# Optimization experiments

Hardware: AMD Instinct MI355X
Metric: run time of the kernel (lower is better)

The kernel has to match this reference:

```python
import jax, jax.numpy as jnp
import numpy as np

T, B, NI, NH = 512, 64, 1024, 1024
SIGMA = 0.01

def setup_inputs() -> dict:
    key = jax.random.key(0)
    ks = jax.random.split(key, 9)
    inputs = jax.random.normal(ks[0], (T, B, NI), dtype=jnp.float32)
    def w(k, shape):
        return jax.random.normal(k, shape, dtype=jnp.float32) * SIGMA
    return {
        "inputs": inputs,
        "W_xf": w(ks[1], (NI, NH)), "W_hf": w(ks[2], (NH, NH)), "b_f": jnp.zeros((NH,), jnp.float32),
        "W_xi": w(ks[3], (NI, NH)), "W_hi": w(ks[4], (NH, NH)), "b_i": jnp.zeros((NH,), jnp.float32),
        "W_xc": w(ks[5], (NI, NH)), "W_hc": w(ks[6], (NH, NH)), "b_c": jnp.zeros((NH,), jnp.float32),
        "W_xo": w(ks[7], (NI, NH)), "W_ho": w(ks[8], (NH, NH)), "b_o": jnp.zeros((NH,), jnp.float32),
    }

def reference(inputs, W_xf, W_hf, b_f, W_xi, W_hi, b_i, W_xc, W_hc, b_c, W_xo, W_ho, b_o):
    # Precompute input projections for all 4 gates in one batched GEMM each:
    # [T,B,NI] @ [NI,4*NH] -> [T,B,4*NH]
    W_x = jnp.concatenate([W_xf, W_xi, W_xc, W_xo], axis=1)
    W_h = jnp.concatenate([W_hf, W_hi, W_hc, W_ho], axis=1)
    b = jnp.concatenate([b_f, b_i, b_c, b_o])
    x_proj = jnp.einsum('tbi,ih->tbh', inputs, W_x) + b  # [T,B,4*NH]

    H0 = jnp.zeros((inputs.shape[1], W_hf.shape[0]), inputs.dtype)
    C0 = jnp.zeros_like(H0)

    def step(carry, xp):
        H, C = carry
        gates = xp + H @ W_h  # [B, 4*NH]
        f, i, c_t, o = jnp.split(gates, 4, axis=-1)
        F = jax.nn.sigmoid(f)
        I = jax.nn.sigmoid(i)
        C_tilde = jnp.tanh(c_t)
        O = jax.nn.sigmoid(o)
        C_new = F * C + I * C_tilde
        H_new = O * jnp.tanh(C_new)
        return (H_new, C_new), H_new

    (H, C), outputs = jax.lax.scan(step, (H0, C0), x_proj)
    return outputs, (H, C)
```

## Files before the change

### kernel.cpp

```cpp
#include <hip/hip_runtime.h>
#include <hip/hip_bf16.h>

#define TT  512
#define BB  64
#define NII 1024
#define NHH 1024
#define NBLK 256

typedef __attribute__((ext_vector_type(8))) short bf16x8;
typedef __attribute__((ext_vector_type(4))) float f32x4;
typedef unsigned long long u64;

#define WPK_BYTES  (16ull << 20)
#define FLG_BYTES  (16384ull)
#define HPP_BYTES  (256ull << 10)
#define XPK_BYTES  (64ull << 20)
#define GX_BYTES   (256ull << 20)
#define HBUF_SHORTS 32768ull

#define MFMA16 __builtin_amdgcn_mfma_f32_16x16x32_bf16
#define LD_AG(p)    __hip_atomic_load((p),  __ATOMIC_RELAXED, __HIP_MEMORY_SCOPE_AGENT)
#define ST_AG(p, v) __hip_atomic_store((p), (v), __ATOMIC_RELAXED, __HIP_MEMORY_SCOPE_AGENT)

__device__ __forceinline__ float fast_sigmoid(float x) {
    return __builtin_amdgcn_rcpf(1.0f + __expf(-x));
}
__device__ __forceinline__ float fast_tanh(float x) {
    float e = __expf(2.0f * x);
    return 1.0f - 2.0f * __builtin_amdgcn_rcpf(e + 1.0f);
}
__device__ __forceinline__ short f2bf(float f) {
    union { __hip_bfloat16 b; short s; } u; u.b = __float2bfloat16(f); return u.s;
}
__device__ __forceinline__ float bf2f(short h) {
    union { unsigned u; float f; } v; v.u = ((unsigned)(unsigned short)h) << 16; return v.f;
}

__device__ __forceinline__ bf16x8 ld_coh16(const short* p) {
    const u64* q = (const u64*)p;
    u64 a = LD_AG(q);
    u64 b = LD_AG(q + 1);
    union { u64 u[2]; bf16x8 v; } u;
    u.u[0] = a; u.u[1] = b; return u.v;
}

__global__ __launch_bounds__(256)
void pack_weights_kernel(const float* __restrict__ Wxf, const float* __restrict__ Whf,
                         const float* __restrict__ Wxi, const float* __restrict__ Whi,
                         const float* __restrict__ Wxc, const float* __restrict__ Whc,
                         const float* __restrict__ Wxo, const float* __restrict__ Who,
                         short* __restrict__ wpk)
{
    const int c = blockIdx.x;
    const int t = threadIdx.x;
    const float* Wx[4] = { Wxf, Wxi, Wxc, Wxo };
    const float* Wh[4] = { Whf, Whi, Whc, Who };

    for (int i = 0; i < 32; ++i) {
        const int d   = t + i * 256;
        const int kkf = d >> 7;
        const int nt  = (d >> 6) & 1;
        const int l   = d & 63;
        const int n   = nt * 16 + (l & 15);
        const int g   = n >> 3;
        const int col = c * 8 + (n & 7);
        const int kf0 = kkf * 32 + (l >> 4) * 8;
        const float* src = (kf0 < 1024) ? (Wx[g] + (size_t)kf0 * NHH + col)
                                        : (Wh[g] + (size_t)(kf0 - 1024) * NHH + col);
        short v[8];
        #pragma unroll
        for (int e = 0; e < 8; ++e) v[e] = f2bf(src[(size_t)e * NHH]);
        *reinterpret_cast<bf16x8*>(wpk + ((size_t)c * 8192 + d) * 8) =
            *reinterpret_cast<bf16x8*>(v);
    }
}

__global__ __launch_bounds__(256)
void pack_x_kernel(const float* __restrict__ x, short* __restrict__ xpk)
{
    const int t = blockIdx.x;
    const float* xt = x + (size_t)t * BB * NII;
    short* dst = xpk + (size_t)t * 65536;

    for (int i = 0; i < 32; ++i) {
        const int d  = threadIdx.x + i * 256;
        const int s  = d >> 12;
        const int mi = (d >> 11) & 1;
        const int kk = (d >> 6) & 31;
        const int l  = d & 63;
        const int m  = s * 32 + mi * 16 + (l & 15);
        const int k0 = kk * 32 + ((l >> 4) << 3);
        const float* sp = xt + (size_t)m * NII + k0;
        f32x4 a0 = *reinterpret_cast<const f32x4*>(sp);
        f32x4 a1 = *reinterpret_cast<const f32x4*>(sp + 4);
        short v[8];
        #pragma unroll
        for (int e = 0; e < 4; ++e) { v[e] = f2bf(a0[e]); v[4 + e] = f2bf(a1[e]); }
        *reinterpret_cast<bf16x8*>(dst + (size_t)d * 8) = *reinterpret_cast<bf16x8*>(v);
    }
}

__global__ __launch_bounds__(256)
void xproj_gemm(const short* __restrict__ xpk, const short* __restrict__ wpk,
                short* __restrict__ gx)
{
    __shared__ short lds_wx[32768];

    const int tid = threadIdx.x;
    const int w = tid >> 6, l = tid & 63;
    const int cp = blockIdx.x & 127, tg = blockIdx.x >> 7;
    const int s = w >> 1, mi = w & 1;

    const short* src = wpk + (size_t)cp * 65536;
    #pragma unroll
    for (int i = 0; i < 16; ++i) {
        const int ch = tid + i * 256;
        *reinterpret_cast<bf16x8*>(&lds_wx[(size_t)ch * 8]) =
            *reinterpret_cast<const bf16x8*>(&src[(size_t)ch * 8]);
    }
    __syncthreads();

    for (int tt = 0; tt < 64; ++tt) {
        const int t = tg * 64 + tt;
        const short* ap = xpk + (size_t)t * 65536
                        + ((size_t)((s * 2 + mi) * 32) * 64 + l) * 8;
        f32x4 a00 = {0,0,0,0}, a01 = {0,0,0,0}, a10 = {0,0,0,0}, a11 = {0,0,0,0};
        const short* wl = &lds_wx[(size_t)l * 8];
        #pragma unroll 4
        for (int kk = 0; kk < 32; kk += 2) {
            bf16x8 A0  = *reinterpret_cast<const bf16x8*>(ap);
            bf16x8 B00 = *reinterpret_cast<const bf16x8*>(wl);
            bf16x8 B01 = *reinterpret_cast<const bf16x8*>(wl + 512);
            bf16x8 A1  = *reinterpret_cast<const bf16x8*>(ap + 512);
            bf16x8 B10 = *reinterpret_cast<const bf16x8*>(wl + 1024);
            bf16x8 B11 = *reinterpret_cast<const bf16x8*>(wl + 1536);
            a00 = MFMA16(A0, B00, a00, 0, 0, 0);
            a01 = MFMA16(A0, B01, a01, 0, 0, 0);
            a10 = MFMA16(A1, B10, a10, 0, 0, 0);
            a11 = MFMA16(A1, B11, a11, 0, 0, 0);
            ap += 1024; wl += 2048;
        }
        short o[8];
        o[0] = f2bf(a00[0] + a10[0]); o[1] = f2bf(a00[1] + a10[1]);
        o[2] = f2bf(a00[2] + a10[2]); o[3] = f2bf(a00[3] + a10[3]);
        o[4] = f2bf(a01[0] + a11[0]); o[5] = f2bf(a01[1] + a11[1]);
        o[6] = f2bf(a01[2] + a11[2]); o[7] = f2bf(a01[3] + a11[3]);
        short* dst = gx + ((((size_t)t * 2 + s) * 128 + cp) * 2 + mi) * 512
                   + (size_t)l * 8;
        *reinterpret_cast<bf16x8*>(dst) = *reinterpret_cast<bf16x8*>(o);
    }
}

__device__ __forceinline__ void compute_x_half(
    int t, int mi, int l, int s, int use_xpk,
    const float* __restrict__ x, const short* __restrict__ xpk,
    const short* lds_w, float* rdst)
{
    f32x4 a00 = {0,0,0,0}, a01 = {0,0,0,0}, a10 = {0,0,0,0}, a11 = {0,0,0,0};
    const short* wl = lds_w + (size_t)l * 8;
    if (use_xpk) {
        const short* ap = xpk + (size_t)t * 65536
                        + (((size_t)(s * 2 + mi)) * 32) * 512 + (size_t)l * 8;
        #pragma unroll 4
        for (int kk = 0; kk < 32; kk += 2) {
            bf16x8 A0  = *reinterpret_cast<const bf16x8*>(ap);
            bf16x8 B00 = *reinterpret_cast<const bf16x8*>(wl);
            bf16x8 B01 = *reinterpret_cast<const bf16x8*>(wl + 512);
            bf16x8 A1  = *reinterpret_cast<const bf16x8*>(ap + 512);
            bf16x8 B10 = *reinterpret_cast<const bf16x8*>(wl + 1024);
            bf16x8 B11 = *reinterpret_cast<const bf16x8*>(wl + 1536);
            a00 = MFMA16(A0, B00, a00, 0, 0, 0);
            a01 = MFMA16(A0, B01, a01, 0, 0, 0);
            a10 = MFMA16(A1, B10, a10, 0, 0, 0);
            a11 = MFMA16(A1, B11, a11, 0, 0, 0);
            ap += 1024; wl += 2048;
        }
    } else {
        const float* apf = x + ((size_t)t * BB + (size_t)(s * 32 + mi * 16 + (l & 15))) * NII
                         + ((l >> 4) << 3);
        #pragma unroll 4
        for (int kk = 0; kk < 32; kk += 2) {
            f32x4 f0 = *reinterpret_cast<const f32x4*>(apf);
            f32x4 f1 = *reinterpret_cast<const f32x4*>(apf + 4);
            bf16x8 B00 = *reinterpret_cast<const bf16x8*>(wl);
            bf16x8 B01 = *reinterpret_cast<const bf16x8*>(wl + 512);
            f32x4 f2 = *reinterpret_cast<const f32x4*>(apf + 32);
            f32x4 f3 = *reinterpret_cast<const f32x4*>(apf + 36);
            bf16x8 B10 = *reinterpret_cast<const bf16x8*>(wl + 1024);
            bf16x8 B11 = *reinterpret_cast<const bf16x8*>(wl + 1536);
            bf16x8 A0, A1;
            A0[0]=f2bf(f0[0]); A0[1]=f2bf(f0[1]); A0[2]=f2bf(f0[2]); A0[3]=f2bf(f0[3]);
            A0[4]=f2bf(f1[0]); A0[5]=f2bf(f1[1]); A0[6]=f2bf(f1[2]); A0[7]=f2bf(f1[3]);
            A1[0]=f2bf(f2[0]); A1[1]=f2bf(f2[1]); A1[2]=f2bf(f2[2]); A1[3]=f2bf(f2[3]);
            A1[4]=f2bf(f3[0]); A1[5]=f2bf(f3[1]); A1[6]=f2bf(f3[2]); A1[7]=f2bf(f3[3]);
            a00 = MFMA16(A0, B00, a00, 0, 0, 0);
            a01 = MFMA16(A0, B01, a01, 0, 0, 0);
            a10 = MFMA16(A1, B10, a10, 0, 0, 0);
            a11 = MFMA16(A1, B11, a11, 0, 0, 0);
            apf += 64; wl += 2048;
        }
    }
    rdst[0] = a00[0] + a10[0]; rdst[1] = a00[1] + a10[1];
    rdst[2] = a00[2] + a10[2]; rdst[3] = a00[3] + a10[3];
    rdst[4] = a01[0] + a11[0]; rdst[5] = a01[1] + a11[1];
    rdst[6] = a01[2] + a11[2]; rdst[7] = a01[3] + a11[3];
}

__global__ __launch_bounds__(256, 1)
void lstm_persistent(const float* __restrict__ x,
                     const short* __restrict__ xpk,
                     const short* __restrict__ wpk,
                     const short* __restrict__ gx,
                     const float* __restrict__ bfv, const float* __restrict__ biv,
                     const float* __restrict__ bcv, const float* __restrict__ bov,
                     float* __restrict__ out,
                     short* hpp,
                     short* ring,
                     unsigned* flags,
                     int mode)
{
    __shared__ short lds_w[64 * 2 * 64 * 8];
    __shared__ float redx[2][2][64][8];
    __shared__ float redh[4][64][8];
    __shared__ short hstage[256];
    __shared__ int   lds_epoch;

    const int tid = threadIdx.x;
    const int w   = tid >> 6;
    const int l   = tid & 63;
    const int c   = blockIdx.x >> 1;
    const int s   = blockIdx.x & 1;

    unsigned* flags_s = flags + s * 2048;

    if (mode == 2) {
        const short* wsrc = wpk + (size_t)c * 65536 + 32768;
        #pragma unroll
        for (int i = 0; i < 16; ++i) {
            const int ch = tid + i * 256;
            *reinterpret_cast<bf16x8*>(&lds_w[(size_t)ch * 8]) =
                *reinterpret_cast<const bf16x8*>(&wsrc[(size_t)ch * 8]);
        }
    } else {
        const short* wsrc = wpk + (size_t)c * 65536;
        #pragma unroll
        for (int i = 0; i < 32; ++i) {
            const int ch = tid + i * 256;
            *reinterpret_cast<bf16x8*>(&lds_w[(size_t)ch * 8]) =
                *reinterpret_cast<const bf16x8*>(&wsrc[(size_t)ch * 8]);
        }
    }
    if (tid == 0) lds_epoch = -1;

    const int m_loc = tid >> 3;
    const int jc    = tid & 7;
    const int mi2   = m_loc >> 4, ml = m_loc & 15;
    const int lb    = (ml >> 2) << 4, lr = ml & 3;
    const int jcol  = c * 8 + jc;
    const int mrow  = s * 32 + m_loc;
    int lanes[4], es[4];
    #pragma unroll
    for (int g = 0; g < 4; ++g) { lanes[g] = lb + (g & 1) * 8 + jc; es[g] = (g >> 1) * 4 + lr; }

    float B4[4];
    B4[0] = bfv[jcol]; B4[1] = biv[jcol]; B4[2] = bcv[jcol]; B4[3] = bov[jcol];
    float cstate = 0.0f;
    __syncthreads();

    float gxv[4] = {0.f, 0.f, 0.f, 0.f};
    if (mode == 2) {
        const short* gsl = gx + ((((size_t)0 * 2 + s) * 128 + c) * 2 + mi2) * 512;
        #pragma unroll
        for (int g = 0; g < 4; ++g) gxv[g] = bf2f(gsl[(size_t)lanes[g] * 8 + es[g]]);
    } else if (w < 2) {
        compute_x_half(0, w & 1, l, s, mode, x, xpk, lds_w, &redx[0][w & 1][l][0]);
    }

    #pragma unroll 1
    for (int t = 0; t < TT; ++t) {
        const short* rcur = (mode == 2)
            ? ring + (size_t)t * 65536 + (size_t)s * 32768
            : hpp + ((size_t)((t & 1) * 2 + s)) * HBUF_SHORTS;
        short* rnxt = (mode == 2)
            ? ring + (size_t)(t + 1) * 65536 + (size_t)s * 32768
            : hpp + ((size_t)(((t + 1) & 1) * 2 + s)) * HBUF_SHORTS;

        if (mode == 2) {
            if (w == 2) {
                const unsigned tv = (unsigned)t;
                for (;;) {
                    unsigned v0 = LD_AG(flags_s + (size_t)l * 16);
                    unsigned v1 = LD_AG(flags_s + (size_t)(l + 64) * 16);
                    if (__all((v0 >= tv) & (v1 >= tv))) break;
                    __builtin_amdgcn_s_sleep(1);
                }
                if (l == 0) *((volatile int*)&lds_epoch) = t;
            } else {
                while (*((volatile int*)&lds_epoch) < t) { }
            }
            asm volatile("" ::: "memory");

            const int mi = w & 1, ki = w >> 1;
            f32x4 a00 = {0,0,0,0}, a01 = {0,0,0,0}, a10 = {0,0,0,0}, a11 = {0,0,0,0};
            const short* ap = rcur + ((size_t)(mi * 32 + ki * 16) * 64 + l) * 8;
            const short* wl = &lds_w[(size_t)ki * 16384 + (size_t)l * 8];
            #pragma unroll 4
            for (int kk = 0; kk < 16; kk += 2) {
                bf16x8 A0  = *reinterpret_cast<const bf16x8*>(ap);
                bf16x8 B00 = *reinterpret_cast<const bf16x8*>(wl);
                bf16x8 B01 = *reinterpret_cast<const bf16x8*>(wl + 512);
                bf16x8 A1  = *reinterpret_cast<const bf16x8*>(ap + 512);
                bf16x8 B10 = *reinterpret_cast<const bf16x8*>(wl + 1024);
                bf16x8 B11 = *reinterpret_cast<const bf16x8*>(wl + 1536);
                a00 = MFMA16(A0, B00, a00, 0, 0, 0);
                a01 = MFMA16(A0, B01, a01, 0, 0, 0);
                a10 = MFMA16(A1, B10, a10, 0, 0, 0);
                a11 = MFMA16(A1, B11, a11, 0, 0, 0);
                ap += 1024; wl += 2048;
            }
            float* r = &redh[w][l][0];
            r[0] = a00[0] + a10[0]; r[1] = a00[1] + a10[1];
            r[2] = a00[2] + a10[2]; r[3] = a00[3] + a10[3];
            r[4] = a01[0] + a11[0]; r[5] = a01[1] + a11[1];
            r[6] = a01[2] + a11[2]; r[7] = a01[3] + a11[3];
        } else if (w >= 2) {
            const int mi = w & 1;
            if (mi == 0) {
                const unsigned tv = (unsigned)t;
                for (;;) {
                    unsigned v0 = LD_AG(flags_s + (size_t)l * 16);
                    unsigned v1 = LD_AG(flags_s + (size_t)(l + 64) * 16);
                    if (__all((v0 >= tv) & (v1 >= tv))) break;
                    __builtin_amdgcn_s_sleep(1);
                }
                if (l == 0) *((volatile int*)&lds_epoch) = t;
            } else {
                while (*((volatile int*)&lds_epoch) < t) { }
            }
            asm volatile("" ::: "memory");

            f32x4 a00 = {0,0,0,0}, a01 = {0,0,0,0}, a10 = {0,0,0,0}, a11 = {0,0,0,0};
            const short* ap = rcur + ((size_t)(mi * 32)) * 512 + (size_t)l * 8;
            const short* wl = &lds_w[(size_t)32768 + (size_t)l * 8];
            #pragma unroll 4
            for (int kk = 0; kk < 32; kk += 2) {
                bf16x8 A0  = ld_coh16(ap);
                bf16x8 B00 = *reinterpret_cast<const bf16x8*>(wl);
                bf16x8 B01 = *reinterpret_cast<const bf16x8*>(wl + 512);
                bf16x8 A1  = ld_coh16(ap + 512);
                bf16x8 B10 = *reinterpret_cast<const bf16x8*>(wl + 1024);
                bf16x8 B11 = *reinterpret_cast<const bf16x8*>(wl + 1536);
                a00 = MFMA16(A0, B00, a00, 0, 0, 0);
                a01 = MFMA16(A0, B01, a01, 0, 0, 0);
                a10 = MFMA16(A1, B10, a10, 0, 0, 0);
                a11 = MFMA16(A1, B11, a11, 0, 0, 0);
                ap += 1024; wl += 2048;
            }
            float* r = &redh[2 + mi][l][0];
            r[0] = a00[0] + a10[0]; r[1] = a00[1] + a10[1];
            r[2] = a00[2] + a10[2]; r[3] = a00[3] + a10[3];
            r[4] = a01[0] + a11[0]; r[5] = a01[1] + a11[1];
            r[6] = a01[2] + a11[2]; r[7] = a01[3] + a11[3];
        } else {
            if (t + 1 < TT)
                compute_x_half(t + 1, w & 1, l, s, mode, x, xpk, lds_w,
                               &redx[(t + 1) & 1][w & 1][l][0]);
        }
        __syncthreads();

        float gv[4];
        #pragma unroll
        for (int g = 0; g < 4; ++g) {
            const int lane = lanes[g], e = es[g];
            float xterm = (mode == 2) ? (gxv[g] + redh[mi2][lane][e])
                                      : redx[t & 1][mi2][lane][e];
            gv[g] = xterm + redh[2 + mi2][lane][e] + B4[g];
        }
        const float F  = fast_sigmoid(gv[0]);
        const float I  = fast_sigmoid(gv[1]);
        const float Ct = fast_tanh(gv[2]);
        const float O  = fast_sigmoid(gv[3]);
        cstate = F * cstate + I * Ct;
        const float hn = O * fast_tanh(cstate);
        hstage[tid] = f2bf(hn);
        __syncthreads();

        if (w == 0 && t < TT - 1) {
            if (l < 32) {
                const int mi3 = l >> 4, ml3 = l & 15;
                const u64 v0 = ((const u64*)hstage)[l * 2];
                const u64 v1 = ((const u64*)hstage)[l * 2 + 1];
                const size_t sh = ((size_t)(mi3 * 32 + (c >> 2)) * 64
                                   + (size_t)((c & 3) * 16 + ml3)) * 8;
                u64* dq = (u64*)(rnxt + sh);
                ST_AG(dq, v0);
                ST_AG(dq + 1, v1);
            }
            asm volatile("s_waitcnt vmcnt(0)" ::: "memory");
            if (tid == 0)
                ST_AG(&flags_s[(size_t)c * 16], (unsigned)(t + 1));
        }

        __builtin_nontemporal_store(hn, &out[(size_t)t * BB * NHH + (size_t)mrow * NHH + jcol]);
        if (t == TT - 1) {
            float* tail = out + (size_t)TT * BB * NHH;
            tail[(size_t)mrow * NHH + jcol]                    = hn;
            tail[(size_t)BB * NHH + (size_t)mrow * NHH + jcol] = cstate;
        }

        if (mode == 2 && t + 1 < TT) {
            const short* gsl = gx + ((((size_t)(t + 1) * 2 + s) * 128 + c) * 2 + mi2) * 512;
            #pragma unroll
            for (int g = 0; g < 4; ++g) gxv[g] = bf2f(gsl[(size_t)lanes[g] * 8 + es[g]]);
        }
    }
}

extern "C" void kernel_launch(void* const* d_in, const int* in_sizes, int n_in,
                              void* d_out, int out_size, void* d_ws, size_t ws_size,
                              hipStream_t stream) {
    const float* inputs = (const float*)d_in[0];
    const float* Wxf = (const float*)d_in[1],  *Whf = (const float*)d_in[2],  *bf = (const float*)d_in[3];
    const float* Wxi = (const float*)d_in[4],  *Whi = (const float*)d_in[5],  *bi = (const float*)d_in[6];
    const float* Wxc = (const float*)d_in[7],  *Whc = (const float*)d_in[8],  *bc = (const float*)d_in[9];
    const float* Wxo = (const float*)d_in[10], *Who = (const float*)d_in[11], *bo = (const float*)d_in[12];

    float* out = (float*)d_out;
    char*  wsb = (char*)d_ws;

    short*    wpk   = (short*)wsb;
    unsigned* flags = (unsigned*)(wsb + WPK_BYTES);
    short*    hpp   = (short*)(wsb + WPK_BYTES + FLG_BYTES);
    short*    xpk   = (short*)(wsb + WPK_BYTES + FLG_BYTES + HPP_BYTES);
    short*    gx    = (short*)(wsb + WPK_BYTES + FLG_BYTES + HPP_BYTES + XPK_BYTES);

    const size_t needT1 = WPK_BYTES + FLG_BYTES + HPP_BYTES + XPK_BYTES;
    const size_t needT0 = needT1 + GX_BYTES;
    const int mode = (ws_size >= needT0) ? 2 : (ws_size >= needT1) ? 1 : 0;

    hipMemsetAsync(flags, 0, FLG_BYTES + HPP_BYTES, stream);

    pack_weights_kernel<<<dim3(128), dim3(256), 0, stream>>>(
        Wxf, Whf, Wxi, Whi, Wxc, Whc, Wxo, Who, wpk);

    if (mode >= 1)
        pack_x_kernel<<<dim3(TT), dim3(256), 0, stream>>>(inputs, xpk);

    if (mode == 2) {
        xproj_gemm<<<dim3(1024), dim3(256), 0, stream>>>(xpk, wpk, gx);
        hipMemsetAsync(xpk, 0, 131072, stream);
    }

    lstm_persistent<<<dim3(NBLK), dim3(256), 0, stream>>>(
        inputs, xpk, wpk, gx, bf, bi, bc, bo, out, hpp, xpk , flags, mode);
}
```

Measured before the change: 2.754 ms.

## Fuse input projection into persistent LSTM kernel with 8-step lookahead ring

Removes the separate xproj_gemm pass and its large gx buffer. The persistent kernel instead computes the input projection for step t+8 after each recurrent step, using all four waves, global-memory W_x slices and an 8-deep LDS ring placed after the weights. The h ring moves into its own workspace region instead of reusing xpk, so mode 2 now needs a smaller workspace. The aim is to hide the x-projection GEMM inside slack in the latency-bound recurrence. The cost is extra per-step work on the serial critical path and global-memory weight reads, since W_x is not held in LDS.

```diff
diff --git a/kernel.cpp b/kernel.cpp
--- a/kernel.cpp
+++ b/kernel.cpp
@@ -15,7 +15,7 @@
 #define FLG_BYTES  (16384ull)
 #define HPP_BYTES  (256ull << 10)
 #define XPK_BYTES  (64ull << 20)
-#define GX_BYTES   (256ull << 20)
+#define RING_BYTES (64ull << 20)
 #define HBUF_SHORTS 32768ull
 
 #define MFMA16 __builtin_amdgcn_mfma_f32_16x16x32_bf16
@@ -31,9 +31,6 @@
 }
 __device__ __forceinline__ short f2bf(float f) {
     union { __hip_bfloat16 b; short s; } u; u.b = __float2bfloat16(f); return u.s;
-}
-__device__ __forceinline__ float bf2f(short h) {
-    union { unsigned u; float f; } v; v.u = ((unsigned)(unsigned short)h) << 16; return v.f;
 }
 
 __device__ __forceinline__ bf16x8 ld_coh16(const short* p) {
@@ -97,57 +94,6 @@
         #pragma unroll
         for (int e = 0; e < 4; ++e) { v[e] = f2bf(a0[e]); v[4 + e] = f2bf(a1[e]); }
         *reinterpret_cast<bf16x8*>(dst + (size_t)d * 8) = *reinterpret_cast<bf16x8*>(v);
-    }
-}
-
-__global__ __launch_bounds__(256)
-void xproj_gemm(const short* __restrict__ xpk, const short* __restrict__ wpk,
-                short* __restrict__ gx)
-{
-    __shared__ short lds_wx[32768];
-
-    const int tid = threadIdx.x;
-    const int w = tid >> 6, l = tid & 63;
-    const int cp = blockIdx.x & 127, tg = blockIdx.x >> 7;
-    const int s = w >> 1, mi = w & 1;
-
-    const short* src = wpk + (size_t)cp * 65536;
-    #pragma unroll
-    for (int i = 0; i < 16; ++i) {
-        const int ch = tid + i * 256;
-        *reinterpret_cast<bf16x8*>(&lds_wx[(size_t)ch * 8]) =
-            *reinterpret_cast<const bf16x8*>(&src[(size_t)ch * 8]);
-    }
-    __syncthreads();
-
-    for (int tt = 0; tt < 64; ++tt) {
-        const int t = tg * 64 + tt;
-        const short* ap = xpk + (size_t)t * 65536
-                        + ((size_t)((s * 2 + mi) * 32) * 64 + l) * 8;
-        f32x4 a00 = {0,0,0,0}, a01 = {0,0,0,0}, a10 = {0,0,0,0}, a11 = {0,0,0,0};
-        const short* wl = &lds_wx[(size_t)l * 8];
-        #pragma unroll 4
-        for (int kk = 0; kk < 32; kk += 2) {
-            bf16x8 A0  = *reinterpret_cast<const bf16x8*>(ap);
-            bf16x8 B00 = *reinterpret_cast<const bf16x8*>(wl);
-            bf16x8 B01 = *reinterpret_cast<const bf16x8*>(wl + 512);
-            bf16x8 A1  = *reinterpret_cast<const bf16x8*>(ap + 512);
-            bf16x8 B10 = *reinterpret_cast<const bf16x8*>(wl + 1024);
-            bf16x8 B11 = *reinterpret_cast<const bf16x8*>(wl + 1536);
-            a00 = MFMA16(A0, B00, a00, 0, 0, 0);
-            a01 = MFMA16(A0, B01, a01, 0, 0, 0);
-            a10 = MFMA16(A1, B10, a10, 0, 0, 0);
-            a11 = MFMA16(A1, B11, a11, 0, 0, 0);
-            ap += 1024; wl += 2048;
-        }
-        short o[8];
-        o[0] = f2bf(a00[0] + a10[0]); o[1] = f2bf(a00[1] + a10[1]);
-        o[2] = f2bf(a00[2] + a10[2]); o[3] = f2bf(a00[3] + a10[3]);
-        o[4] = f2bf(a01[0] + a11[0]); o[5] = f2bf(a01[1] + a11[1]);
-        o[6] = f2bf(a01[2] + a11[2]); o[7] = f2bf(a01[3] + a11[3]);
-        short* dst = gx + ((((size_t)t * 2 + s) * 128 + cp) * 2 + mi) * 512
-                   + (size_t)l * 8;
-        *reinterpret_cast<bf16x8*>(dst) = *reinterpret_cast<bf16x8*>(o);
     }
 }
 
@@ -206,11 +152,39 @@
     rdst[6] = a01[2] + a11[2]; rdst[7] = a01[3] + a11[3];
 }
 
+__device__ __forceinline__ void compute_x_ki(
+    int t, int mi, int ki, int l, int s,
+    const short* __restrict__ xpk, const short* __restrict__ wxc,
+    float* rdst)
+{
+    f32x4 a00 = {0,0,0,0}, a01 = {0,0,0,0}, a10 = {0,0,0,0}, a11 = {0,0,0,0};
+    const short* ap = xpk + (size_t)t * 65536
+                    + ((size_t)((s * 2 + mi) * 32 + ki * 16)) * 512 + (size_t)l * 8;
+    const short* wl = wxc + (size_t)ki * 16384 + (size_t)l * 8;
+    #pragma unroll 4
+    for (int kk = 0; kk < 16; kk += 2) {
+        bf16x8 A0  = *reinterpret_cast<const bf16x8*>(ap);
+        bf16x8 B00 = *reinterpret_cast<const bf16x8*>(wl);
+        bf16x8 B01 = *reinterpret_cast<const bf16x8*>(wl + 512);
+        bf16x8 A1  = *reinterpret_cast<const bf16x8*>(ap + 512);
+        bf16x8 B10 = *reinterpret_cast<const bf16x8*>(wl + 1024);
+        bf16x8 B11 = *reinterpret_cast<const bf16x8*>(wl + 1536);
+        a00 = MFMA16(A0, B00, a00, 0, 0, 0);
+        a01 = MFMA16(A0, B01, a01, 0, 0, 0);
+        a10 = MFMA16(A1, B10, a10, 0, 0, 0);
+        a11 = MFMA16(A1, B11, a11, 0, 0, 0);
+        ap += 1024; wl += 2048;
+    }
+    rdst[0] = a00[0] + a10[0]; rdst[1] = a00[1] + a10[1];
+    rdst[2] = a00[2] + a10[2]; rdst[3] = a00[3] + a10[3];
+    rdst[4] = a01[0] + a11[0]; rdst[5] = a01[1] + a11[1];
+    rdst[6] = a01[2] + a11[2]; rdst[7] = a01[3] + a11[3];
+}
+
 __global__ __launch_bounds__(256, 1)
 void lstm_persistent(const float* __restrict__ x,
                      const short* __restrict__ xpk,
                      const short* __restrict__ wpk,
-                     const short* __restrict__ gx,
                      const float* __restrict__ bfv, const float* __restrict__ biv,
                      const float* __restrict__ bcv, const float* __restrict__ bov,
                      float* __restrict__ out,
@@ -228,10 +202,14 @@
     const int tid = threadIdx.x;
     const int w   = tid >> 6;
     const int l   = tid & 63;
+    const int mi  = w & 1;
+    const int ki  = w >> 1;
     const int c   = blockIdx.x >> 1;
     const int s   = blockIdx.x & 1;
 
     unsigned* flags_s = flags + s * 2048;
+    float (*redxr)[4][64][8] = (float (*)[4][64][8])(lds_w + 32768);
+    const short* wxc = wpk + (size_t)c * 65536;
 
     if (mode == 2) {
         const short* wsrc = wpk + (size_t)c * 65536 + 32768;
@@ -267,14 +245,13 @@
     float cstate = 0.0f;
     __syncthreads();
 
-    float gxv[4] = {0.f, 0.f, 0.f, 0.f};
     if (mode == 2) {
-        const short* gsl = gx + ((((size_t)0 * 2 + s) * 128 + c) * 2 + mi2) * 512;
-        #pragma unroll
-        for (int g = 0; g < 4; ++g) gxv[g] = bf2f(gsl[(size_t)lanes[g] * 8 + es[g]]);
+        for (int tp = 0; tp < 8; ++tp)
+            compute_x_ki(tp, mi, ki, l, s, xpk, wxc, &redxr[tp][w][l][0]);
     } else if (w < 2) {
-        compute_x_half(0, w & 1, l, s, mode, x, xpk, lds_w, &redx[0][w & 1][l][0]);
-    }
+        compute_x_half(0, mi, l, s, mode, x, xpk, lds_w, &redx[0][mi][l][0]);
+    }
+    __syncthreads();
 
     #pragma unroll 1
     for (int t = 0; t < TT; ++t) {
@@ -300,7 +277,6 @@
             }
             asm volatile("" ::: "memory");
 
-            const int mi = w & 1, ki = w >> 1;
             f32x4 a00 = {0,0,0,0}, a01 = {0,0,0,0}, a10 = {0,0,0,0}, a11 = {0,0,0,0};
             const short* ap = rcur + ((size_t)(mi * 32 + ki * 16) * 64 + l) * 8;
             const short* wl = &lds_w[(size_t)ki * 16384 + (size_t)l * 8];
@@ -324,7 +300,6 @@
             r[4] = a01[0] + a11[0]; r[5] = a01[1] + a11[1];
             r[6] = a01[2] + a11[2]; r[7] = a01[3] + a11[3];
         } else if (w >= 2) {
-            const int mi = w & 1;
             if (mi == 0) {
                 const unsigned tv = (unsigned)t;
                 for (;;) {
@@ -363,8 +338,8 @@
             r[6] = a01[2] + a11[2]; r[7] = a01[3] + a11[3];
         } else {
             if (t + 1 < TT)
-                compute_x_half(t + 1, w & 1, l, s, mode, x, xpk, lds_w,
-                               &redx[(t + 1) & 1][w & 1][l][0]);
+                compute_x_half(t + 1, mi, l, s, mode, x, xpk, lds_w,
+                               &redx[(t + 1) & 1][mi][l][0]);
         }
         __syncthreads();
 
@@ -372,8 +347,12 @@
         #pragma unroll
         for (int g = 0; g < 4; ++g) {
             const int lane = lanes[g], e = es[g];
-            float xterm = (mode == 2) ? (gxv[g] + redh[mi2][lane][e])
-                                      : redx[t & 1][mi2][lane][e];
+            float xterm;
+            if (mode == 2)
+                xterm = redxr[t & 7][mi2][lane][e] + redxr[t & 7][2 + mi2][lane][e]
+                      + redh[mi2][lane][e];
+            else
+                xterm = redx[t & 1][mi2][lane][e];
             gv[g] = xterm + redh[2 + mi2][lane][e] + B4[g];
         }
         const float F  = fast_sigmoid(gv[0]);
@@ -408,11 +387,9 @@
             tail[(size_t)BB * NHH + (size_t)mrow * NHH + jcol] = cstate;
         }
 
-        if (mode == 2 && t + 1 < TT) {
-            const short* gsl = gx + ((((size_t)(t + 1) * 2 + s) * 128 + c) * 2 + mi2) * 512;
-            #pragma unroll
-            for (int g = 0; g < 4; ++g) gxv[g] = bf2f(gsl[(size_t)lanes[g] * 8 + es[g]]);
-        }
+        if (mode == 2 && t + 8 < TT)
+            compute_x_ki(t + 8, mi, ki, l, s, xpk, wxc,
+                         &redxr[(t + 8) & 7][w][l][0]);
     }
 }
 
@@ -432,13 +409,15 @@
     unsigned* flags = (unsigned*)(wsb + WPK_BYTES);
     short*    hpp   = (short*)(wsb + WPK_BYTES + FLG_BYTES);
     short*    xpk   = (short*)(wsb + WPK_BYTES + FLG_BYTES + HPP_BYTES);
-    short*    gx    = (short*)(wsb + WPK_BYTES + FLG_BYTES + HPP_BYTES + XPK_BYTES);
+    short*    ring  = (short*)(wsb + WPK_BYTES + FLG_BYTES + HPP_BYTES + XPK_BYTES);
 
     const size_t needT1 = WPK_BYTES + FLG_BYTES + HPP_BYTES + XPK_BYTES;
-    const size_t needT0 = needT1 + GX_BYTES;
-    const int mode = (ws_size >= needT0) ? 2 : (ws_size >= needT1) ? 1 : 0;
+    const size_t needT2 = needT1 + RING_BYTES;
+    const int mode = (ws_size >= needT2) ? 2 : (ws_size >= needT1) ? 1 : 0;
 
     hipMemsetAsync(flags, 0, FLG_BYTES + HPP_BYTES, stream);
+    if (mode == 2)
+        hipMemsetAsync(ring, 0, 131072, stream);
 
     pack_weights_kernel<<<dim3(128), dim3(256), 0, stream>>>(
         Wxf, Whf, Wxi, Whi, Wxc, Whc, Wxo, Who, wpk);
@@ -446,11 +425,6 @@
     if (mode >= 1)
         pack_x_kernel<<<dim3(TT), dim3(256), 0, stream>>>(inputs, xpk);
 
-    if (mode == 2) {
-        xproj_gemm<<<dim3(1024), dim3(256), 0, stream>>>(xpk, wpk, gx);
-        hipMemsetAsync(xpk, 0, 131072, stream);
-    }
-
     lstm_persistent<<<dim3(NBLK), dim3(256), 0, stream>>>(
-        inputs, xpk, wpk, gx, bf, bi, bc, bo, out, hpp, xpk , flags, mode);
-}
+        inputs, xpk, wpk, bf, bi, bc, bo, out, hpp, ring, flags, mode);
+}
```

New measurement: 3.047 ms. +10.6%, slower.
